# Optimization experiments

Hardware: AMD Instinct MI355X
Metric: run time of the kernel (lower is better)

## Reference

```python
import jax, jax.numpy as jnp
import numpy as np

B, N, E, H, SD, HID = 4, 512, 1024, 16, 64, 64
D = E // H  # head_dim


def setup_inputs() -> dict:
    key = jax.random.key(0)
    ks = jax.random.split(key, 20)
    s = lambda i, shape, scale: (jax.random.normal(ks[i], shape, dtype=jnp.float32) * scale)
    inp = {
        "query": s(0, (B, N, E), 1.0),
        "key": s(1, (B, N, E), 1.0),
        "value": s(2, (B, N, E), 1.0),
        "state_embeddings": s(3, (B, N, SD), 1.0),
        # projection weights stored [in, out] (transposed vs torch nn.Linear)
        "Wq": s(4, (E, E), E ** -0.5), "bq": jnp.zeros((E,), jnp.float32),
        "Wk": s(5, (E, E), E ** -0.5), "bk": jnp.zeros((E,), jnp.float32),
        "Wv": s(6, (E, E), E ** -0.5), "bv": jnp.zeros((E,), jnp.float32),
        "Wo": s(7, (E, E), E ** -0.5), "bo": jnp.zeros((E,), jnp.float32),
        # CAB compatibility MLP: Linear(2*SD->HID), ReLU, Linear(HID->HID), ReLU, Linear(HID->H)
        "W1": s(8, (2 * SD, HID), (2 * SD) ** -0.5), "b1": jnp.zeros((HID,), jnp.float32),
        "W2": s(9, (HID, HID), HID ** -0.5), "b2": jnp.zeros((HID,), jnp.float32),
        "W3": s(10, (HID, H), HID ** -0.5), "b3": jnp.zeros((H,), jnp.float32),
        "head_temps": jnp.ones((H,), jnp.float32),
    }
    return inp


def reference(query, key, value, state_embeddings,
              Wq, bq, Wk, bk, Wv, bv, Wo, bo,
              W1, b1, W2, b2, W3, b3, head_temps):
    scale = D ** -0.5
    q = (query @ Wq + bq).reshape(B, N, H, D)
    k = (key @ Wk + bk).reshape(B, N, H, D)
    v = (value @ Wv + bv).reshape(B, N, H, D)
    # [B, H, T, S]
    scores = jnp.einsum("bthd,bshd->bhts", q, k) * scale

    # CAB bias: MLP([e_i; e_j]) -> split first layer to avoid materializing pairs
    hi = state_embeddings @ W1[:SD]          # [B, N, HID]
    hj = state_embeddings @ W1[SD:]          # [B, N, HID]
    h = jax.nn.relu(hi[:, :, None, :] + hj[:, None, :, :] + b1)  # [B, N, N, HID]
    h = jax.nn.relu(h @ W2 + b2)
    comp = h @ W3 + b3                        # [B, N, N, H]
    bias = jnp.transpose(comp, (0, 3, 1, 2)) * head_temps[None, :, None, None]
    scores = scores + bias

    attn = jax.nn.softmax(scores, axis=-1)
    out = jnp.einsum("bhts,bshd->bthd", attn, v).reshape(B, N, E)
    return out @ Wo + bo
```

## Files before the change

kernel.cpp:

```cpp
#include <hip/hip_runtime.h>
#include <hip/hip_bf16.h>

typedef unsigned short u16;
typedef short short8 __attribute__((ext_vector_type(8)));
typedef float f32x4 __attribute__((ext_vector_type(4)));
typedef unsigned short u16x4 __attribute__((ext_vector_type(4)));

#define BB 4
#define NS 512
#define EE 1024
#define HH 16
#define DD 64
#define MM (BB*NS)
#define NSQ 2
#define SQW (NS/NSQ)

__device__ __forceinline__ u16 f2bfh(float x) {
  __hip_bfloat16 h = __float2bfloat16(x);
  union { __hip_bfloat16 h; u16 u; } c; c.h = h; return c.u;
}
__device__ __forceinline__ unsigned pkbf(float a, float b) {
  union { __hip_bfloat16 h; u16 u; } ca, cb;
  ca.h = __float2bfloat16(a); cb.h = __float2bfloat16(b);
  return (unsigned)ca.u | ((unsigned)cb.u << 16);
}
union S8 { short8 s; unsigned u[4]; };

__device__ __forceinline__ void gload_lds16(const void* g, void* l) {
  __builtin_amdgcn_global_load_lds(
      (const __attribute__((address_space(1))) unsigned int*)g,
      (__attribute__((address_space(3))) unsigned int*)l, 16, 0, 0);
}


__global__ void cvt_w(const float* __restrict__ Wq, const float* __restrict__ Wk,
                      const float* __restrict__ Wv, const float* __restrict__ Wo,
                      const float* __restrict__ W2, const float* __restrict__ W3,
                      const float* __restrict__ q, const float* __restrict__ k,
                      const float* __restrict__ v,
                      u16* __restrict__ WqT, u16* __restrict__ WkT,
                      u16* __restrict__ WvT, u16* __restrict__ WoT,
                      u16* __restrict__ W2T, u16* __restrict__ W3P,
                      u16* __restrict__ qb, u16* __restrict__ kb, u16* __restrict__ vb) {
  int z = blockIdx.z;
  if (z >= 5) {
    int seg = z - 5;
    const float* src = seg == 0 ? q : (seg == 1 ? k : v);
    u16* dst = seg == 0 ? qb : (seg == 1 ? kb : vb);
    size_t flat = ((size_t)blockIdx.y * 32 + blockIdx.x) * 256 + threadIdx.x;
    size_t off = flat << 3;
    float4 f0 = *(const float4*)(src + off);
    float4 f1 = *(const float4*)(src + off + 4);
    S8 r;
    r.u[0] = pkbf(f0.x, f0.y); r.u[1] = pkbf(f0.z, f0.w);
    r.u[2] = pkbf(f1.x, f1.y); r.u[3] = pkbf(f1.z, f1.w);
    *(short8*)(dst + off) = r.s;
    return;
  }
  if (z == 4) {
    if (blockIdx.x || blockIdx.y) return;
    int tid = threadIdx.x;
    for (int i = tid; i < 4096; i += 256) {
      int n = i >> 6, kk = i & 63;
      W2T[i] = f2bfh(W2[kk * 64 + n]);
    }
    for (int i = tid; i < 1024; i += 256) {
      int h = i >> 6, rem = i & 63;
      int k2 = rem >> 5, gg = (rem >> 3) & 3, j = rem & 7;
      int c = (2 * k2 + (j >> 2)) * 16 + gg * 4 + (j & 3);
      W3P[i] = f2bfh(W3[c * 16 + h]);
    }
    return;
  }
  const float* W = z == 0 ? Wq : z == 1 ? Wk : z == 2 ? Wv : Wo;
  u16* WT = z == 0 ? WqT : z == 1 ? WkT : z == 2 ? WvT : WoT;
  int n0 = blockIdx.x << 5, k0 = blockIdx.y << 5;
  __shared__ float tile[32][33];
  int tx = threadIdx.x & 31, ty = threadIdx.x >> 5;
  #pragma unroll
  for (int i = 0; i < 4; ++i) {
    int r = (i << 3) + ty;
    tile[r][tx] = W[(size_t)(k0 + r) * EE + n0 + tx];
  }
  __syncthreads();
  #pragma unroll
  for (int i = 0; i < 4; ++i) {
    int r = (i << 3) + ty;
    WT[(size_t)(n0 + r) * EE + k0 + tx] = f2bfh(tile[tx][r]);
  }
}


__global__ void hi_hj_kernel(const float* __restrict__ se, const float* __restrict__ W1,
                             const float* __restrict__ b1,
                             float* __restrict__ hi, float* __restrict__ hj) {
  int tid = threadIdx.x;
  int row = blockIdx.x * 4 + (tid >> 6);
  int c = tid & 63;
  float ah = b1[c], aj = 0.f;
  #pragma unroll 8
  for (int k = 0; k < 64; ++k) {
    float s = se[row * 64 + k];
    ah += s * W1[k * 64 + c];
    aj += s * W1[(k + 64) * 64 + c];
  }
  hi[row * 64 + c] = ah;
  hj[row * 64 + c] = aj;
}


template <int MODE>
__device__ __forceinline__ void gemm_body(const u16* __restrict__ A, const u16* __restrict__ Bt,
                                          const float* __restrict__ bias, void* __restrict__ Cout) {
  __shared__ u16 As[128 * 32];
  __shared__ u16 Bs[128 * 32];
  const int tid = threadIdx.x, lane = tid & 63, wave = tid >> 6;
  const int m0 = blockIdx.x * 128, n0 = blockIdx.y * 128;
  const int wr = wave >> 1, wc = wave & 1;

  const f32x4 zero = {0.f, 0.f, 0.f, 0.f};
  f32x4 acc[4][4];
  #pragma unroll
  for (int i = 0; i < 4; ++i)
    #pragma unroll
    for (int j = 0; j < 4; ++j) acc[i][j] = zero;

  const int rA = lane >> 2;
  const int cA = (lane & 3) << 3;

  for (int kt = 0; kt < EE; kt += 32) {
    #pragma unroll
    for (int i = 0; i < 2; ++i) {
      int base = ((i << 2) + wave) << 9;
      int row = (base >> 5) + rA;
      gload_lds16(A  + (size_t)(m0 + row) * EE + kt + cA, As + base);
      gload_lds16(Bt + (size_t)(n0 + row) * EE + kt + cA, Bs + base);
    }
    __syncthreads();
    short8 af[4], bfr[4];
    #pragma unroll
    for (int mf = 0; mf < 4; ++mf) {
      int row = wr * 64 + mf * 16 + (lane & 15);
      af[mf] = *(const short8*)(As + row * 32 + ((lane >> 4) << 3));
    }
    #pragma unroll
    for (int nf = 0; nf < 4; ++nf) {
      int row = wc * 64 + nf * 16 + (lane & 15);
      bfr[nf] = *(const short8*)(Bs + row * 32 + ((lane >> 4) << 3));
    }
    #pragma unroll
    for (int mf = 0; mf < 4; ++mf)
      #pragma unroll
      for (int nf = 0; nf < 4; ++nf)
        acc[mf][nf] = __builtin_amdgcn_mfma_f32_16x16x32_bf16(af[mf], bfr[nf], acc[mf][nf], 0, 0, 0);
    __syncthreads();
  }

  #pragma unroll
  for (int mf = 0; mf < 4; ++mf) {
    #pragma unroll
    for (int nf = 0; nf < 4; ++nf) {
      int col = n0 + wc * 64 + nf * 16 + (lane & 15);
      float bv = bias[col];
      #pragma unroll
      for (int j = 0; j < 4; ++j) {
        int rowm = m0 + wr * 64 + mf * 16 + ((lane >> 4) << 2) + j;
        float v = acc[mf][nf][j] + bv;
        int bb = rowm >> 9, r = rowm & 511;
        int h = col >> 6, d = col & 63;
        size_t off;
        if (MODE == 0)
          off = ((((size_t)bb * HH + h) * 32 + (r >> 4)) << 10) + ((size_t)(d >> 5) << 9)
              + ((size_t)((((d >> 3) & 3) << 4) + (r & 15)) << 3) + (d & 7);
        else
          off = (((((size_t)bb * HH + h) * 16 + (r >> 5)) * 4 + (d >> 4)) << 9)
              + ((size_t)((((r >> 3) & 3) << 4) + (d & 15)) << 3) + (r & 7);
        ((u16*)Cout)[off] = f2bfh(v);
      }
    }
  }
}

__global__ __launch_bounds__(256, 2) void gemm_proj(
    const u16* __restrict__ qb, const u16* __restrict__ kb, const u16* __restrict__ vb,
    const u16* __restrict__ WqT, const u16* __restrict__ WkT, const u16* __restrict__ WvT,
    const float* __restrict__ bq, const float* __restrict__ bk, const float* __restrict__ bv_,
    u16* __restrict__ qF, u16* __restrict__ kF, u16* __restrict__ vF) {
  int z = blockIdx.z;
  if (z == 0)      gemm_body<0>(qb, WqT, bq, qF);
  else if (z == 1) gemm_body<0>(kb, WkT, bk, kF);
  else             gemm_body<1>(vb, WvT, bv_, vF);
}


__global__ __launch_bounds__(256, 2) void gemm_final64(
    const u16* __restrict__ A, const u16* __restrict__ Bt,
    const float* __restrict__ bias, float* __restrict__ C) {
  __shared__ u16 As[64 * 32];
  __shared__ u16 Bs[128 * 32];
  const int tid = threadIdx.x, lane = tid & 63, wave = tid >> 6;
  const int m0 = blockIdx.x * 64, n0 = blockIdx.y * 128;
  const int wr = wave >> 1, wc = wave & 1;

  const f32x4 zero = {0.f, 0.f, 0.f, 0.f};
  f32x4 acc[2][4];
  #pragma unroll
  for (int i = 0; i < 2; ++i)
    #pragma unroll
    for (int j = 0; j < 4; ++j) acc[i][j] = zero;

  const int rA = lane >> 2;
  const int cA = (lane & 3) << 3;

  for (int kt = 0; kt < EE; kt += 32) {
    {
      int base = wave << 9;
      int row = (wave << 4) + rA;
      gload_lds16(A + (size_t)(m0 + row) * EE + kt + cA, As + base);
    }
    #pragma unroll
    for (int i = 0; i < 2; ++i) {
      int base = ((i << 2) + wave) << 9;
      int row = (base >> 5) + rA;
      gload_lds16(Bt + (size_t)(n0 + row) * EE + kt + cA, Bs + base);
    }
    __syncthreads();
    short8 af[2], bfr[4];
    #pragma unroll
    for (int mf = 0; mf < 2; ++mf) {
      int row = wr * 32 + mf * 16 + (lane & 15);
      af[mf] = *(const short8*)(As + row * 32 + ((lane >> 4) << 3));
    }
    #pragma unroll
    for (int nf = 0; nf < 4; ++nf) {
      int row = wc * 64 + nf * 16 + (lane & 15);
      bfr[nf] = *(const short8*)(Bs + row * 32 + ((lane >> 4) << 3));
    }
    #pragma unroll
    for (int mf = 0; mf < 2; ++mf)
      #pragma unroll
      for (int nf = 0; nf < 4; ++nf)
        acc[mf][nf] = __builtin_amdgcn_mfma_f32_16x16x32_bf16(af[mf], bfr[nf], acc[mf][nf], 0, 0, 0);
    __syncthreads();
  }

  #pragma unroll
  for (int mf = 0; mf < 2; ++mf)
    #pragma unroll
    for (int nf = 0; nf < 4; ++nf) {
      int col = n0 + wc * 64 + nf * 16 + (lane & 15);
      float bv = bias[col];
      #pragma unroll
      for (int j = 0; j < 4; ++j) {
        int rowm = m0 + wr * 32 + mf * 16 + ((lane >> 4) << 2) + j;
        C[(size_t)rowm * EE + col] = acc[mf][nf][j] + bv;
      }
    }
}


__global__ __launch_bounds__(512, 2) void fused_cab_attn(
    const float* __restrict__ hi, const float* __restrict__ hj,
    const u16* __restrict__ W2T, const u16* __restrict__ W3P,
    const float* __restrict__ b2, const float* __restrict__ b3,
    const float* __restrict__ temps,
    const u16* __restrict__ qF, const u16* __restrict__ kF,
    const u16* __restrict__ vF,
    float* __restrict__ Opart, float* __restrict__ mlpart) {
  const int b = blockIdx.x >> 1, sq = blockIdx.x & 1, tt = blockIdx.y;
  const int t0 = tt << 4;
  const int tid = threadIdx.x, lane = tid & 63, wave = tid >> 6;
  const int g = lane >> 4, sl = lane & 15;

  __shared__ float hi_s[16][80];
  __shared__ float hj_s[2][32][65];
  __shared__ float b2_s[64], b3_s[16], tp_s[16];
  __shared__ float comp3[16 * 273];
  __shared__ u16 Pl[8][16][40];

  if (tid < 256) {
    int r = tid >> 4, c4 = (tid & 15) << 2;
    float4 hv = *(const float4*)(hi + ((size_t)(b * NS + t0 + r) << 6) + c4);
    *(f32x4*)&hi_s[r][c4] = (f32x4){hv.x, hv.y, hv.z, hv.w};
  } else {
    int ix = tid - 256;
    if (ix < 64) b2_s[ix] = b2[ix];
    else if (ix < 80) b3_s[ix - 64] = b3[ix - 64];
    else if (ix < 96) tp_s[ix - 80] = temps[ix - 80];
  }

  const int hr = tid >> 4, hc4 = (tid & 15) << 2;
  {
    float4 a = *(const float4*)(hj + ((size_t)(b * NS + sq * SQW + hr) << 6) + hc4);
    hj_s[0][hr][hc4 + 0] = a.x; hj_s[0][hr][hc4 + 1] = a.y;
    hj_s[0][hr][hc4 + 2] = a.z; hj_s[0][hr][hc4 + 3] = a.w;
  }

  const f32x4 zero = {0.f, 0.f, 0.f, 0.f};
  f32x4 acc[2][4];
  #pragma unroll
  for (int i = 0; i < 2; ++i)
    #pragma unroll
    for (int j = 0; j < 4; ++j) acc[i][j] = zero;
  float m_run[2] = {-3e38f, -3e38f};
  float l_run[2] = {0.f, 0.f};

  int cur = 0;
  for (int pr = 0; pr < 8; ++pr) {
    const int s0p = sq * SQW + (pr << 5);
    __syncthreads();

    float4 hjnx;
    const bool have = (pr + 1) < 8;
    if (have)
      hjnx = *(const float4*)(hj + ((size_t)(b * NS + s0p + 32 + hr) << 6) + hc4);

    float vsc[2][2][4];

    #pragma unroll
    for (int ta = 0; ta < 2; ++ta) {
      if (ta) __syncthreads();
      {
        float hjv[2][8];
        #pragma unroll
        for (int kk = 0; kk < 2; ++kk)
          #pragma unroll
          for (int j = 0; j < 8; ++j)
            hjv[kk][j] = hj_s[cur][(ta << 4) + sl][kk * 32 + (g << 3) + j];

        short8 w3f[2];
        #pragma unroll
        for (int k2 = 0; k2 < 2; ++k2)
          w3f[k2] = *(const short8*)(W3P + (sl << 6) + k2 * 32 + (g << 3));

        float b2v[4][4];
        #pragma unroll
        for (int mfc = 0; mfc < 4; ++mfc)
          #pragma unroll
          for (int jj = 0; jj < 4; ++jj)
            b2v[mfc][jj] = b2_s[mfc * 16 + (g << 2) + jj];

        #pragma unroll
        for (int q = 0; q < 2; ++q) {
          int tl = (wave << 1) + q;
          short8 xb[2];
          #pragma unroll
          for (int kk = 0; kk < 2; ++kk) {
            int c0 = kk * 32 + (g << 3);
            f32x4 h0 = *(const f32x4*)&hi_s[tl][c0];
            f32x4 h1 = *(const f32x4*)&hi_s[tl][c0 + 4];
            float x[8];
            #pragma unroll
            for (int j = 0; j < 4; ++j) {
              x[j]     = fmaxf(h0[j] + hjv[kk][j], 0.f);
              x[j + 4] = fmaxf(h1[j] + hjv[kk][j + 4], 0.f);
            }
            S8 r;
            r.u[0] = pkbf(x[0], x[1]); r.u[1] = pkbf(x[2], x[3]);
            r.u[2] = pkbf(x[4], x[5]); r.u[3] = pkbf(x[6], x[7]);
            xb[kk] = r.s;
          }
          f32x4 accY[4];
          #pragma unroll
          for (int i = 0; i < 4; ++i) accY[i] = zero;
          #pragma unroll
          for (int kk = 0; kk < 2; ++kk)
            #pragma unroll
            for (int mfc = 0; mfc < 4; ++mfc) {
              short8 w2 = *(const short8*)(W2T + ((mfc * 16 + sl) << 6) + kk * 32 + (g << 3));
              accY[mfc] = __builtin_amdgcn_mfma_f32_16x16x32_bf16(w2, xb[kk], accY[mfc], 0, 0, 0);
            }
          f32x4 compD = zero;
          #pragma unroll
          for (int k2 = 0; k2 < 2; ++k2) {
            float y[8];
            #pragma unroll
            for (int j = 0; j < 4; ++j) {
              y[j]     = fmaxf(accY[2 * k2][j]     + b2v[2 * k2][j],     0.f);
              y[j + 4] = fmaxf(accY[2 * k2 + 1][j] + b2v[2 * k2 + 1][j], 0.f);
            }
            S8 r;
            r.u[0] = pkbf(y[0], y[1]); r.u[1] = pkbf(y[2], y[3]);
            r.u[2] = pkbf(y[4], y[5]); r.u[3] = pkbf(y[6], y[7]);
            compD = __builtin_amdgcn_mfma_f32_16x16x32_bf16(w3f[k2], r.s, compD, 0, 0, 0);
          }
          #pragma unroll
          for (int jj = 0; jj < 4; ++jj) {
            int h = (g << 2) + jj;
            comp3[h * 273 + sl * 17 + tl] = (compD[jj] + b3_s[h]) * tp_s[h];
          }
        }
      }
      __syncthreads();
      const int s16 = (sq << 4) + (pr << 1) + ta;
      #pragma unroll
      for (int hh = 0; hh < 2; ++hh) {
        int h = (wave << 1) + hh;
        const u16* qb_ = qF + ((((size_t)b * HH + h) * 32 + tt) << 10) + (lane << 3);
        const u16* kb_ = kF + ((((size_t)b * HH + h) * 32 + s16) << 10) + (lane << 3);
        f32x4 accS = zero;
        accS = __builtin_amdgcn_mfma_f32_16x16x32_bf16(*(const short8*)kb_, *(const short8*)qb_, accS, 0, 0, 0);
        accS = __builtin_amdgcn_mfma_f32_16x16x32_bf16(*(const short8*)(kb_ + 512), *(const short8*)(qb_ + 512), accS, 0, 0, 0);
        #pragma unroll
        for (int j = 0; j < 4; ++j)
          vsc[ta][hh][j] = accS[j] * 0.125f + comp3[h * 273 + ((g << 2) + j) * 17 + sl];
      }
    }

    if (have) {
      hj_s[cur ^ 1][hr][hc4 + 0] = hjnx.x; hj_s[cur ^ 1][hr][hc4 + 1] = hjnx.y;
      hj_s[cur ^ 1][hr][hc4 + 2] = hjnx.z; hj_s[cur ^ 1][hr][hc4 + 3] = hjnx.w;
    }

    #pragma unroll
    for (int hh = 0; hh < 2; ++hh) {
      int h = (wave << 1) + hh;
      float e[8];
      float mx = -3e38f;
      #pragma unroll
      for (int j = 0; j < 4; ++j)
        mx = fmaxf(mx, fmaxf(vsc[0][hh][j], vsc[1][hh][j]));
      mx = fmaxf(mx, __shfl_xor(mx, 16, 64));
      mx = fmaxf(mx, __shfl_xor(mx, 32, 64));
      float mnew = fmaxf(m_run[hh], mx);
      float c = __expf(m_run[hh] - mnew);
      m_run[hh] = mnew;
      #pragma unroll
      for (int ta = 0; ta < 2; ++ta)
        #pragma unroll
        for (int j = 0; j < 4; ++j)
          e[ta * 4 + j] = __expf(vsc[ta][hh][j] - mnew);
      float ps = ((e[0] + e[1]) + (e[2] + e[3])) + ((e[4] + e[5]) + (e[6] + e[7]));
      ps += __shfl_xor(ps, 16, 64);
      ps += __shfl_xor(ps, 32, 64);
      l_run[hh] = l_run[hh] * c + ps;

      uint2 wA; wA.x = pkbf(e[0], e[1]); wA.y = pkbf(e[2], e[3]);
      uint2 wB; wB.x = pkbf(e[4], e[5]); wB.y = pkbf(e[6], e[7]);
      *(uint2*)&Pl[wave][sl][(g << 2)]      = wA;
      *(uint2*)&Pl[wave][sl][16 + (g << 2)] = wB;
      short8 pf = *(const short8*)&Pl[wave][sl][(g << 3)];

      float cb[4];
      #pragma unroll
      for (int j = 0; j < 4; ++j) cb[j] = __shfl(c, (g << 2) + j, 64);

      const u16* vb0 = vF + (((((size_t)b * HH + h) * 16 + (sq << 3) + pr) * 4) << 9) + (lane << 3);
      #pragma unroll
      for (int nf = 0; nf < 4; ++nf) {
        #pragma unroll
        for (int j = 0; j < 4; ++j) acc[hh][nf][j] *= cb[j];
        short8 vv = *(const short8*)(vb0 + ((size_t)nf << 9));
        acc[hh][nf] = __builtin_amdgcn_mfma_f32_16x16x32_bf16(pf, vv, acc[hh][nf], 0, 0, 0);
      }
    }
    cur ^= 1;
  }

  size_t obase = ((size_t)sq * MM + (size_t)b * NS + t0) * EE;
  #pragma unroll
  for (int hh = 0; hh < 2; ++hh) {
    int h = (wave << 1) + hh;
    #pragma unroll
    for (int nf = 0; nf < 4; ++nf)
      #pragma unroll
      for (int j = 0; j < 4; ++j)
        Opart[obase + (size_t)((g << 2) + j) * EE + (h << 6) + nf * 16 + sl] = acc[hh][nf][j];
  }
  if (g == 0) {
    #pragma unroll
    for (int hh = 0; hh < 2; ++hh) {
      int h = (wave << 1) + hh;
      size_t mlb = (((size_t)sq * MM + b * NS + t0 + sl) * HH + h) * 2;
      mlpart[mlb] = m_run[hh];
      mlpart[mlb + 1] = l_run[hh];
    }
  }
}


__global__ void combine_pv(const float* __restrict__ Opart, const float* __restrict__ mlpart,
                           u16* __restrict__ attn_out) {
  int row = blockIdx.x;
  int tid = threadIdx.x;
  int c4 = tid << 2;
  int h = c4 >> 6;
  float m[NSQ], l[NSQ];
  #pragma unroll
  for (int pq = 0; pq < NSQ; ++pq) {
    size_t mb = (((size_t)pq * MM + row) * HH + h) * 2;
    m[pq] = mlpart[mb]; l[pq] = mlpart[mb + 1];
  }
  float M = m[0];
  #pragma unroll
  for (int pq = 1; pq < NSQ; ++pq) M = fmaxf(M, m[pq]);
  float den = 0.f;
  f32x4 num = {0.f, 0.f, 0.f, 0.f};
  #pragma unroll
  for (int pq = 0; pq < NSQ; ++pq) {
    float w = __expf(m[pq] - M);
    den += w * l[pq];
    f32x4 o = *(const f32x4*)(Opart + ((size_t)pq * MM + row) * EE + c4);
    #pragma unroll
    for (int i = 0; i < 4; ++i) num[i] += w * o[i];
  }
  float r = 1.0f / den;
  u16x4 out;
  #pragma unroll
  for (int i = 0; i < 4; ++i) out[i] = f2bfh(num[i] * r);
  *(u16x4*)(attn_out + (size_t)row * EE + c4) = out;
}


extern "C" void kernel_launch(void* const* d_in, const int* in_sizes, int n_in,
                              void* d_out, int out_size, void* d_ws, size_t ws_size,
                              hipStream_t stream) {
  const float* query = (const float*)d_in[0];
  const float* key   = (const float*)d_in[1];
  const float* value = (const float*)d_in[2];
  const float* se    = (const float*)d_in[3];
  const float* Wq = (const float*)d_in[4];  const float* bq = (const float*)d_in[5];
  const float* Wk = (const float*)d_in[6];  const float* bk = (const float*)d_in[7];
  const float* Wv = (const float*)d_in[8];  const float* bv = (const float*)d_in[9];
  const float* Wo = (const float*)d_in[10]; const float* bo = (const float*)d_in[11];
  const float* W1 = (const float*)d_in[12]; const float* b1 = (const float*)d_in[13];
  const float* W2 = (const float*)d_in[14]; const float* b2 = (const float*)d_in[15];
  const float* W3 = (const float*)d_in[16]; const float* b3 = (const float*)d_in[17];
  const float* temps = (const float*)d_in[18];

  char* p = (char*)d_ws;
  auto alloc = [&](size_t bytes) { char* r = p; p += (bytes + 255) & ~(size_t)255; return r; };
  u16* qb  = (u16*)alloc((size_t)MM * EE * 2);
  u16* kb  = (u16*)alloc((size_t)MM * EE * 2);
  u16* vb  = (u16*)alloc((size_t)MM * EE * 2);
  u16* WqT = (u16*)alloc((size_t)EE * EE * 2);
  u16* WkT = (u16*)alloc((size_t)EE * EE * 2);
  u16* WvT = (u16*)alloc((size_t)EE * EE * 2);
  u16* WoT = (u16*)alloc((size_t)EE * EE * 2);
  u16* W2T = (u16*)alloc(4096 * 2);
  u16* W3P = (u16*)alloc(1024 * 2);
  u16* qF  = (u16*)alloc((size_t)MM * EE * 2);
  u16* kF  = (u16*)alloc((size_t)MM * EE * 2);
  u16* vF  = (u16*)alloc((size_t)MM * EE * 2);
  float* hi = (float*)alloc((size_t)MM * 64 * 4);
  float* hj = (float*)alloc((size_t)MM * 64 * 4);
  float* Opart = (float*)alloc((size_t)NSQ * MM * EE * 4);
  float* mlpart = (float*)alloc((size_t)NSQ * MM * HH * 2 * 4);
  u16* attn_out = (u16*)alloc((size_t)MM * EE * 2);
  (void)ws_size; (void)in_sizes; (void)n_in; (void)out_size;

  cvt_w<<<dim3(32, 32, 8), 256, 0, stream>>>(Wq, Wk, Wv, Wo, W2, W3, query, key, value,
                                             WqT, WkT, WvT, WoT, W2T, W3P, qb, kb, vb);
  hi_hj_kernel<<<512, 256, 0, stream>>>(se, W1, b1, hi, hj);
  gemm_proj<<<dim3(16, 8, 3), 256, 0, stream>>>(qb, kb, vb, WqT, WkT, WvT, bq, bk, bv, qF, kF, vF);
  fused_cab_attn<<<dim3(8, 32, 1), 512, 0, stream>>>(hi, hj, W2T, W3P, b2, b3, temps,
                                                     qF, kF, vF, Opart, mlpart);
  combine_pv<<<MM, 256, 0, stream>>>(Opart, mlpart, attn_out);
  gemm_final64<<<dim3(32, 8), 256, 0, stream>>>(attn_out, WoT, bo, (float*)d_out);
}
```

Before: 114.9 us.

## Split key dimension four ways with 256-thread blocks in fused CAB attention

Raises the key-sequence split from 2 to 4 and halves the block to 4 waves, each handling 4 heads and 4 query rows. The grid doubles to 512 blocks, giving more blocks to spread across CUs, and each block's serial loop is shorter. The cost is twice the partial-output traffic to Opart, more work in combine_pv, and more registers per thread for the larger accumulator arrays.

```diff
diff --git a/kernel.cpp b/kernel.cpp
--- a/kernel.cpp
+++ b/kernel.cpp
@@ -12,8 +12,9 @@
 #define HH 16
 #define DD 64
 #define MM (BB*NS)
-#define NSQ 2
+#define NSQ 4
 #define SQW (NS/NSQ)
+#define NPR (SQW/32)
 
 __device__ __forceinline__ u16 f2bfh(float x) {
   __hip_bfloat16 h = __float2bfloat16(x);
@@ -259,7 +260,7 @@
 }
 
 
-__global__ __launch_bounds__(512, 2) void fused_cab_attn(
+__global__ __launch_bounds__(256, 2) void fused_cab_attn(
     const float* __restrict__ hi, const float* __restrict__ hj,
     const u16* __restrict__ W2T, const u16* __restrict__ W3P,
     const float* __restrict__ b2, const float* __restrict__ b3,
@@ -267,7 +268,9 @@
     const u16* __restrict__ qF, const u16* __restrict__ kF,
     const u16* __restrict__ vF,
     float* __restrict__ Opart, float* __restrict__ mlpart) {
-  const int b = blockIdx.x >> 1, sq = blockIdx.x & 1, tt = blockIdx.y;
+  const int b = blockIdx.x >> 1, sqlo = blockIdx.x & 1;
+  const int tt = blockIdx.y >> 1, sqhi = blockIdx.y & 1;
+  const int sq = (sqhi << 1) | sqlo;
   const int t0 = tt << 4;
   const int tid = threadIdx.x, lane = tid & 63, wave = tid >> 6;
   const int g = lane >> 4, sl = lane & 15;
@@ -276,46 +279,51 @@
   __shared__ float hj_s[2][32][65];
   __shared__ float b2_s[64], b3_s[16], tp_s[16];
   __shared__ float comp3[16 * 273];
-  __shared__ u16 Pl[8][16][40];
-
-  if (tid < 256) {
+  __shared__ u16 Pl[4][16][40];
+
+  {
     int r = tid >> 4, c4 = (tid & 15) << 2;
     float4 hv = *(const float4*)(hi + ((size_t)(b * NS + t0 + r) << 6) + c4);
     *(f32x4*)&hi_s[r][c4] = (f32x4){hv.x, hv.y, hv.z, hv.w};
-  } else {
-    int ix = tid - 256;
-    if (ix < 64) b2_s[ix] = b2[ix];
-    else if (ix < 80) b3_s[ix - 64] = b3[ix - 64];
-    else if (ix < 96) tp_s[ix - 80] = temps[ix - 80];
-  }
-
-  const int hr = tid >> 4, hc4 = (tid & 15) << 2;
+    if (tid < 64) b2_s[tid] = b2[tid];
+    else if (tid < 80) b3_s[tid - 64] = b3[tid - 64];
+    else if (tid < 96) tp_s[tid - 80] = temps[tid - 80];
+  }
+
+  const int hr = tid >> 3, hc8 = (tid & 7) << 3;
   {
-    float4 a = *(const float4*)(hj + ((size_t)(b * NS + sq * SQW + hr) << 6) + hc4);
-    hj_s[0][hr][hc4 + 0] = a.x; hj_s[0][hr][hc4 + 1] = a.y;
-    hj_s[0][hr][hc4 + 2] = a.z; hj_s[0][hr][hc4 + 3] = a.w;
+    const float* src = hj + ((size_t)(b * NS + sq * SQW + hr) << 6) + hc8;
+    float4 a0 = *(const float4*)src;
+    float4 a1 = *(const float4*)(src + 4);
+    hj_s[0][hr][hc8 + 0] = a0.x; hj_s[0][hr][hc8 + 1] = a0.y;
+    hj_s[0][hr][hc8 + 2] = a0.z; hj_s[0][hr][hc8 + 3] = a0.w;
+    hj_s[0][hr][hc8 + 4] = a1.x; hj_s[0][hr][hc8 + 5] = a1.y;
+    hj_s[0][hr][hc8 + 6] = a1.z; hj_s[0][hr][hc8 + 7] = a1.w;
   }
 
   const f32x4 zero = {0.f, 0.f, 0.f, 0.f};
-  f32x4 acc[2][4];
-  #pragma unroll
-  for (int i = 0; i < 2; ++i)
+  f32x4 acc[4][4];
+  #pragma unroll
+  for (int i = 0; i < 4; ++i)
     #pragma unroll
     for (int j = 0; j < 4; ++j) acc[i][j] = zero;
-  float m_run[2] = {-3e38f, -3e38f};
-  float l_run[2] = {0.f, 0.f};
+  float m_run[4] = {-3e38f, -3e38f, -3e38f, -3e38f};
+  float l_run[4] = {0.f, 0.f, 0.f, 0.f};
 
   int cur = 0;
-  for (int pr = 0; pr < 8; ++pr) {
+  for (int pr = 0; pr < NPR; ++pr) {
     const int s0p = sq * SQW + (pr << 5);
     __syncthreads();
 
-    float4 hjnx;
-    const bool have = (pr + 1) < 8;
-    if (have)
-      hjnx = *(const float4*)(hj + ((size_t)(b * NS + s0p + 32 + hr) << 6) + hc4);
-
-    float vsc[2][2][4];
+    float4 hjnx0, hjnx1;
+    const bool have = (pr + 1) < NPR;
+    if (have) {
+      const float* src = hj + ((size_t)(b * NS + s0p + 32 + hr) << 6) + hc8;
+      hjnx0 = *(const float4*)src;
+      hjnx1 = *(const float4*)(src + 4);
+    }
+
+    float vsc[2][4][4];
 
     #pragma unroll
     for (int ta = 0; ta < 2; ++ta) {
@@ -341,8 +349,8 @@
             b2v[mfc][jj] = b2_s[mfc * 16 + (g << 2) + jj];
 
         #pragma unroll
-        for (int q = 0; q < 2; ++q) {
-          int tl = (wave << 1) + q;
+        for (int q = 0; q < 4; ++q) {
+          int tl = (wave << 2) + q;
           short8 xb[2];
           #pragma unroll
           for (int kk = 0; kk < 2; ++kk) {
@@ -392,10 +400,10 @@
         }
       }
       __syncthreads();
-      const int s16 = (sq << 4) + (pr << 1) + ta;
-      #pragma unroll
-      for (int hh = 0; hh < 2; ++hh) {
-        int h = (wave << 1) + hh;
+      const int s16 = (sq << 3) + (pr << 1) + ta;
+      #pragma unroll
+      for (int hh = 0; hh < 4; ++hh) {
+        int h = (wave << 2) + hh;
         const u16* qb_ = qF + ((((size_t)b * HH + h) * 32 + tt) << 10) + (lane << 3);
         const u16* kb_ = kF + ((((size_t)b * HH + h) * 32 + s16) << 10) + (lane << 3);
         f32x4 accS = zero;
@@ -408,13 +416,15 @@
     }
 
     if (have) {
-      hj_s[cur ^ 1][hr][hc4 + 0] = hjnx.x; hj_s[cur ^ 1][hr][hc4 + 1] = hjnx.y;
-      hj_s[cur ^ 1][hr][hc4 + 2] = hjnx.z; hj_s[cur ^ 1][hr][hc4 + 3] = hjnx.w;
-    }
-
-    #pragma unroll
-    for (int hh = 0; hh < 2; ++hh) {
-      int h = (wave << 1) + hh;
+      hj_s[cur ^ 1][hr][hc8 + 0] = hjnx0.x; hj_s[cur ^ 1][hr][hc8 + 1] = hjnx0.y;
+      hj_s[cur ^ 1][hr][hc8 + 2] = hjnx0.z; hj_s[cur ^ 1][hr][hc8 + 3] = hjnx0.w;
+      hj_s[cur ^ 1][hr][hc8 + 4] = hjnx1.x; hj_s[cur ^ 1][hr][hc8 + 5] = hjnx1.y;
+      hj_s[cur ^ 1][hr][hc8 + 6] = hjnx1.z; hj_s[cur ^ 1][hr][hc8 + 7] = hjnx1.w;
+    }
+
+    #pragma unroll
+    for (int hh = 0; hh < 4; ++hh) {
+      int h = (wave << 2) + hh;
       float e[8];
       float mx = -3e38f;
       #pragma unroll
@@ -445,7 +455,7 @@
       #pragma unroll
       for (int j = 0; j < 4; ++j) cb[j] = __shfl(c, (g << 2) + j, 64);
 
-      const u16* vb0 = vF + (((((size_t)b * HH + h) * 16 + (sq << 3) + pr) * 4) << 9) + (lane << 3);
+      const u16* vb0 = vF + (((((size_t)b * HH + h) * 16 + (sq << 2) + pr) * 4) << 9) + (lane << 3);
       #pragma unroll
       for (int nf = 0; nf < 4; ++nf) {
         #pragma unroll
@@ -459,8 +469,8 @@
 
   size_t obase = ((size_t)sq * MM + (size_t)b * NS + t0) * EE;
   #pragma unroll
-  for (int hh = 0; hh < 2; ++hh) {
-    int h = (wave << 1) + hh;
+  for (int hh = 0; hh < 4; ++hh) {
+    int h = (wave << 2) + hh;
     #pragma unroll
     for (int nf = 0; nf < 4; ++nf)
       #pragma unroll
@@ -469,8 +479,8 @@
   }
   if (g == 0) {
     #pragma unroll
-    for (int hh = 0; hh < 2; ++hh) {
-      int h = (wave << 1) + hh;
+    for (int hh = 0; hh < 4; ++hh) {
+      int h = (wave << 2) + hh;
       size_t mlb = (((size_t)sq * MM + b * NS + t0 + sl) * HH + h) * 2;
       mlpart[mlb] = m_run[hh];
       mlpart[mlb + 1] = l_run[hh];
@@ -553,7 +563,7 @@
                                              WqT, WkT, WvT, WoT, W2T, W3P, qb, kb, vb);
   hi_hj_kernel<<<512, 256, 0, stream>>>(se, W1, b1, hi, hj);
   gemm_proj<<<dim3(16, 8, 3), 256, 0, stream>>>(qb, kb, vb, WqT, WkT, WvT, bq, bk, bv, qF, kF, vF);
-  fused_cab_attn<<<dim3(8, 32, 1), 512, 0, stream>>>(hi, hj, W2T, W3P, b2, b3, temps,
+  fused_cab_attn<<<dim3(8, 64, 1), 256, 0, stream>>>(hi, hj, W2T, W3P, b2, b3, temps,
                                                      qF, kF, vF, Opart, mlpart);
   combine_pv<<<MM, 256, 0, stream>>>(Opart, mlpart, attn_out);
   gemm_final64<<<dim3(32, 8), 256, 0, stream>>>(attn_out, WoT, bo, (float*)d_out);
```

Result: slower. 138.8 us (+20.8%).
